# Performance work log

Hardware: AMD Instinct MI355X
Metric: run time of the kernel (lower is better)

## Reference

```python
import jax, jax.numpy as jnp
import numpy as np

FACTOR = 5  # sampling factor from __init__


def setup_inputs() -> dict:
    key = jax.random.key(0)
    k1, k2, k3, k4 = jax.random.split(key, 4)
    B, L, H, D = 4, 2048, 8, 64
    S = min(FACTOR * int(np.ceil(np.log(L))), L)  # U_part = 40
    return {
        "queries": jax.random.normal(k1, (B, L, H, D), jnp.float32),
        "keys": jax.random.normal(k2, (B, L, H, D), jnp.float32),
        "values": jax.random.normal(k3, (B, L, H, D), jnp.float32),
        "index_sample": jax.random.randint(k4, (L, S), 0, L, jnp.int32),
    }


def reference(queries, keys, values, index_sample):
    B, L_Q, H, D = queries.shape
    L_K = keys.shape[1]
    Q = jnp.transpose(queries, (0, 2, 1, 3))  # [B,H,L_Q,D]
    K = jnp.transpose(keys, (0, 2, 1, 3))     # [B,H,L_K,D]
    V = jnp.transpose(values, (0, 2, 1, 3))   # [B,H,L_K,D]

    u = min(FACTOR * int(np.ceil(np.log(L_Q))), L_Q)  # n_top

    # --- _prob_QK: sampled QK to score queries, then top-u query selection ---
    # K_sample[b,h,q,s,:] = K[b,h,index_sample[q,s],:]  -> [B,H,L_Q,S,D]
    K_sample = K[:, :, index_sample, :]
    Q_K_sample = jnp.einsum('bhqd,bhqsd->bhqs', Q, K_sample)  # [B,H,L_Q,S]
    M = Q_K_sample.max(-1) - Q_K_sample.sum(-1) / L_K         # sparsity measure
    _, M_top = jax.lax.top_k(M, u)                            # [B,H,u] query indices

    Q_reduce = jnp.take_along_axis(Q, M_top[..., None], axis=2)  # [B,H,u,D]
    scale = 1.0 / np.sqrt(D)
    scores = jnp.einsum('bhud,bhkd->bhuk', Q_reduce, K) * scale  # [B,H,u,L_K]

    # --- _update_context causal mask: rows are the FIRST u rows of the full
    # triu(L_Q,L_Q) mask (faithful to original, which does NOT reindex by M_top)
    causal = jnp.triu(jnp.ones((u, L_Q), dtype=bool), 1)
    scores = jnp.where(causal[None, None], -jnp.inf, scores)
    attn = jax.nn.softmax(scores, axis=-1)
    upd = jnp.einsum('bhuk,bhkd->bhud', attn, V)  # [B,H,u,D]

    # --- _get_initial_context (mask_flag=True): running cumsum of V ---
    context = jnp.cumsum(V, axis=2)  # [B,H,L_Q,D]

    # scatter-overwrite selected query positions
    b = jnp.arange(B)[:, None, None]
    h = jnp.arange(H)[None, :, None]
    context = context.at[b, h, M_top].set(upd)

    return jnp.transpose(context, (0, 2, 1, 3))  # [B,L_Q,H,D]
```

## Files before the change

kernel.cpp:

```cpp
#include <hip/hip_runtime.h>
#include <stdint.h>

constexpr int B = 4;
constexpr int L = 2048;
constexpr int H = 8;
constexpr int D = 64;
constexpr int S = 40;
constexpr int U = 40;
constexpr int HD = H * D;
constexpr int NSEG = 8;
constexpr int SEGL = L / NSEG;
constexpr int NC = 64;
constexpr int CL = L / NC;
constexpr int ROCT = 8;
constexpr int RPO = U / ROCT;

constexpr int NBLK_SCORES = B * L / 4;
constexpr int NBLK_CHUNK  = B * NC;
constexpr int NBLK_FLAG   = 64;

__device__ __forceinline__ unsigned mono(float v) {
    unsigned u = __float_as_uint(v);
    return (u & 0x80000000u) ? ~u : (u | 0x80000000u);
}

typedef float f4v __attribute__((ext_vector_type(4)));

__device__ __forceinline__ float4 ntload4(const float4* p) {
    f4v v = __builtin_nontemporal_load((const f4v*)p);
    return make_float4(v.x, v.y, v.z, v.w);
}

__global__ __launch_bounds__(256) void k_scores_chunks(
    const float4* __restrict__ Q4, const float4* __restrict__ K4,
    const int* __restrict__ idxs, const float* __restrict__ V,
    float* __restrict__ M, float* __restrict__ partial,
    int* __restrict__ flags)
{
    int i = blockIdx.x;

    if (i < NBLK_SCORES) {
        int xcd = i & 7;
        int b = xcd >> 1;
        int qc = (i >> 3) * 2 + (xcd & 1);
        int w = threadIdx.x >> 6;
        int lane = threadIdx.x & 63;
        int q = qc * 4 + w;
        int g = lane >> 4;
        int m = lane & 15;

        const float4* qrow = Q4 + (size_t)(b * L + q) * 128;
        float4 qa = ntload4(qrow + lane);
        float4 qb = ntload4(qrow + 64 + lane);

        int v_idx = idxs[q * S + (lane < S ? lane : 0)];

        const float4* kbase = K4 + (size_t)b * L * 128;
        float mxA = -INFINITY, smA = 0.f;
        float mxB = -INFINITY, smB = 0.f;
        #pragma unroll 8
        for (int s = 0; s < S; ++s) {
            int ki = __shfl(v_idx, s);
            const float4* krow = kbase + (size_t)ki * 128;
            float4 ka = krow[lane];
            float4 kb = krow[64 + lane];
            float dA = qa.x * ka.x + qa.y * ka.y + qa.z * ka.z + qa.w * ka.w;
            float dB = qb.x * kb.x + qb.y * kb.y + qb.z * kb.z + qb.w * kb.w;
            dA += __shfl_xor(dA, 1);  dB += __shfl_xor(dB, 1);
            dA += __shfl_xor(dA, 2);  dB += __shfl_xor(dB, 2);
            dA += __shfl_xor(dA, 4);  dB += __shfl_xor(dB, 4);
            dA += __shfl_xor(dA, 8);  dB += __shfl_xor(dB, 8);
            mxA = fmaxf(mxA, dA);  smA += dA;
            mxB = fmaxf(mxB, dB);  smB += dB;
        }
        if (m == 0) {
            M[(b * 8 + g) * L + q]       = mxA - smA * (1.0f / (float)L);
            M[(b * 8 + g + 4) * L + q]   = mxB - smB * (1.0f / (float)L);
        }
    } else if (i < NBLK_SCORES + NBLK_CHUNK) {
        int cidx = i - NBLK_SCORES;
        int b = cidx >> 6, c = cidx & 63;
        int t = threadIdx.x;
        const float* vp = V + ((size_t)(b * L + c * CL)) * HD;
        float s0 = 0.f, s1 = 0.f;
        #pragma unroll
        for (int l = 0; l < CL; ++l) {
            s0 += __builtin_nontemporal_load(vp + (size_t)l * HD + t);
            s1 += __builtin_nontemporal_load(vp + (size_t)l * HD + t + 256);
        }
        partial[((size_t)b * NC + c) * HD + t]       = s0;
        partial[((size_t)b * NC + c) * HD + t + 256] = s1;
    } else {
        int fidx = i - (NBLK_SCORES + NBLK_CHUNK);
        ((int4*)flags)[fidx * 256 + threadIdx.x] = make_int4(0, 0, 0, 0);
    }
}

__global__ __launch_bounds__(64) void k_seg_topk(
    const float* __restrict__ M, unsigned long long* __restrict__ cand)
{
    int blk = blockIdx.x;
    int bh = blk >> 3, seg = blk & 7;
    int lane = threadIdx.x;
    int j0 = seg * SEGL + lane * 4;

    float4 v = *(const float4*)(M + (size_t)bh * L + j0);
    unsigned m[4] = { mono(v.x), mono(v.y), mono(v.z), mono(v.w) };
    int rank[4] = { 0, 0, 0, 0 };

    #pragma unroll 4
    for (int src = 0; src < 64; ++src) {
        #pragma unroll
        for (int slot = 0; slot < 4; ++slot) {
            unsigned bm = __shfl(m[slot], src);
            int bj = src * 4 + slot;
            #pragma unroll
            for (int s = 0; s < 4; ++s) {
                int myj = lane * 4 + s;
                rank[s] += (bm > m[s]) || (bm == m[s] && bj < myj);
            }
        }
    }

    unsigned long long* out = cand + (size_t)blk * U;
    #pragma unroll
    for (int s = 0; s < 4; ++s)
        if (rank[s] < U)
            out[rank[s]] = ((unsigned long long)m[s] << 32)
                         | (unsigned)(~(unsigned)(j0 + s));
}

__global__ __launch_bounds__(512) void k_attn(
    const unsigned long long* __restrict__ cand, const float4* __restrict__ Q4,
    const float4* __restrict__ K4, const float4* __restrict__ V4,
    int* __restrict__ flags, float* __restrict__ upd)
{
    __shared__ unsigned long long cnd[NSEG * U];
    __shared__ int top_idx[U];
    __shared__ __align__(16) float Qs[RPO * 68];
    __shared__ __align__(16) float Kst[64 * 65];
    __shared__ __align__(16) float Vs[U * 68];
    __shared__ __align__(16) float Plds[RPO * 44];

    int blk = blockIdx.x;
    int bh = blk >> 3, oct = blk & 7;
    int b = bh >> 3, h = bh & 7;
    int tid = threadIdx.x;
    int wv = tid >> 6, lane = tid & 63;

    for (int t = tid; t < NSEG * U; t += 512)
        cnd[t] = cand[(size_t)bh * NSEG * U + t];
    __syncthreads();

    if (tid < NSEG * U) {
        unsigned long long ka = cnd[tid];
        int ra = 0;
        #pragma unroll 8
        for (int j = 0; j < NSEG * U; ++j) ra += (cnd[j] > ka);
        if (ra < U) top_idx[ra] = (int)(~(unsigned)ka);
    }
    __syncthreads();

    if (oct == 0 && tid < U) flags[bh * L + top_idx[tid]] = tid + 1;

    for (int i = tid; i < U * 16; i += 512) {
        int r = i >> 4, d4 = i & 15;
        size_t kvbase = ((size_t)(b * L + r) * H + h) * 16 + d4;
        float4 kv = K4[kvbase];
        Kst[(4 * d4 + 0) * 65 + r] = kv.x;
        Kst[(4 * d4 + 1) * 65 + r] = kv.y;
        Kst[(4 * d4 + 2) * 65 + r] = kv.z;
        Kst[(4 * d4 + 3) * 65 + r] = kv.w;
        *(float4*)(Vs + r * 68 + d4 * 4) = V4[kvbase];
    }
    if (tid < RPO * 16) {
        int rl = tid >> 4, d4 = tid & 15;
        int qg = top_idx[oct * RPO + rl];
        *(float4*)(Qs + rl * 68 + d4 * 4) =
            Q4[((size_t)(b * L + qg) * H + h) * 16 + d4];
    }
    __syncthreads();

    const float scale = 0.125f;
    if (wv < RPO) {
        int rg = oct * RPO + wv;
        int k = lane;
        float acc = 0.f;
        #pragma unroll
        for (int d0 = 0; d0 < D; d0 += 4) {
            float4 qv = *(const float4*)(Qs + wv * 68 + d0);
            acc += qv.x * Kst[(d0 + 0) * 65 + k];
            acc += qv.y * Kst[(d0 + 1) * 65 + k];
            acc += qv.z * Kst[(d0 + 2) * 65 + k];
            acc += qv.w * Kst[(d0 + 3) * 65 + k];
        }
        float sc = (k <= rg) ? acc * scale : -INFINITY;
        float mx = sc;
        #pragma unroll
        for (int off = 32; off >= 1; off >>= 1)
            mx = fmaxf(mx, __shfl_xor(mx, off));
        float e = __expf(sc - mx);
        float sum = e;
        #pragma unroll
        for (int off = 32; off >= 1; off >>= 1)
            sum += __shfl_xor(sum, off);
        float p = e / sum;
        if (k < U) Plds[wv * 44 + k] = p;
    }
    __syncthreads();

    if (tid < RPO * D) {
        int rl = tid >> 6, d = tid & 63;
        float acc = 0.f;
        #pragma unroll
        for (int kk = 0; kk < U; kk += 4) {
            float4 pv = *(const float4*)(Plds + rl * 44 + kk);
            acc += pv.x * Vs[(kk + 0) * 68 + d];
            acc += pv.y * Vs[(kk + 1) * 68 + d];
            acc += pv.z * Vs[(kk + 2) * 68 + d];
            acc += pv.w * Vs[(kk + 3) * 68 + d];
        }
        upd[((size_t)bh * U + oct * RPO + rl) * D + d] = acc;
    }
}

__global__ __launch_bounds__(512) void k_out(
    const float* __restrict__ V, const float* __restrict__ partial,
    const int* __restrict__ flags, const float* __restrict__ upd,
    float* __restrict__ out)
{
    int b = blockIdx.x >> 6;
    int c = blockIdx.x & 63;
    int hd = threadIdx.x;
    int h = hd >> 6, d = hd & 63;

    const float* pp = partial + (size_t)b * NC * HD + hd;
    float a0 = 0.f, a1 = 0.f, a2 = 0.f, a3 = 0.f;
    int j = 0;
    for (; j + 4 <= c; j += 4) {
        a0 += pp[(size_t)(j + 0) * HD];
        a1 += pp[(size_t)(j + 1) * HD];
        a2 += pp[(size_t)(j + 2) * HD];
        a3 += pp[(size_t)(j + 3) * HD];
    }
    for (; j < c; ++j) a0 += pp[(size_t)j * HD];
    float acc = (a0 + a1) + (a2 + a3);

    const float* vp = V + ((size_t)(b * L + c * CL)) * HD + hd;
    float*       op = out + ((size_t)(b * L + c * CL)) * HD + hd;
    const int*   fp = flags + (b * H + h) * L + c * CL;
    const float* up = upd + (size_t)(b * H + h) * U * D + d;

    #pragma unroll 4
    for (int l = 0; l < CL; ++l) {
        acc += vp[(size_t)l * HD];
        int f = fp[l];
        float o = f ? up[(size_t)(f - 1) * D] : acc;
        __builtin_nontemporal_store(o, op + (size_t)l * HD);
    }
}

extern "C" void kernel_launch(void* const* d_in, const int* in_sizes, int n_in,
                              void* d_out, int out_size, void* d_ws, size_t ws_size,
                              hipStream_t stream)
{
    const float* Q   = (const float*)d_in[0];
    const float* K   = (const float*)d_in[1];
    const float* V   = (const float*)d_in[2];
    const int*  idxs = (const int*)d_in[3];
    float* out = (float*)d_out;

    char* ws = (char*)d_ws;
    float* M        = (float*)(ws);
    int*   flags    = (int*)  (ws + 262144);
    float* upd      = (float*)(ws + 524288);
    float* partial  = (float*)(ws + 851968);
    unsigned long long* cand = (unsigned long long*)(ws + 1376256);

    k_scores_chunks<<<NBLK_SCORES + NBLK_CHUNK + NBLK_FLAG, 256, 0, stream>>>(
        (const float4*)Q, (const float4*)K, idxs, V, M, partial, flags);
    k_seg_topk <<<B * H * NSEG, 64, 0, stream>>>(M, cand);
    k_attn     <<<B * H * ROCT, 512, 0, stream>>>(cand, (const float4*)Q, (const float4*)K,
                                                  (const float4*)V, flags, upd);
    k_out      <<<B * NC,      512, 0, stream>>>(V, partial, flags, upd, out);
}
```

Baseline: 174.5 us.

## Fuse segment top-k into attention kernel and split sample loop across waves

The segmented top-k kernel is removed. Each of the 8 attention blocks per (b,h) now recomputes the 8 segment rankings itself from M, one wave per segment, writing candidates straight to shared memory. This drops one kernel launch and the candidate buffer round trip, at the cost of repeating the ranking work 8 times across blocks. Separately, the scoring kernel now splits the 40 samples across two waves per query, combining max and sum through shared memory. This doubles the block count to add memory-level parallelism on the gathered K rows.

```diff
diff --git a/kernel.cpp b/kernel.cpp
--- a/kernel.cpp
+++ b/kernel.cpp
@@ -14,8 +14,9 @@
 constexpr int CL = L / NC;
 constexpr int ROCT = 8;
 constexpr int RPO = U / ROCT;
-
-constexpr int NBLK_SCORES = B * L / 4;
+constexpr int SH = S / 2;
+
+constexpr int NBLK_SCORES = B * L / 2;
 constexpr int NBLK_CHUNK  = B * NC;
 constexpr int NBLK_FLAG   = 64;
 
@@ -31,7 +32,7 @@
     return make_float4(v.x, v.y, v.z, v.w);
 }
 
-__global__ __launch_bounds__(256) void k_scores_chunks(
+__global__ __launch_bounds__(256, 4) void k_scores_chunks(
     const float4* __restrict__ Q4, const float4* __restrict__ K4,
     const int* __restrict__ idxs, const float* __restrict__ V,
     float* __restrict__ M, float* __restrict__ partial,
@@ -40,12 +41,16 @@
     int i = blockIdx.x;
 
     if (i < NBLK_SCORES) {
+        __shared__ float red_mx[4][8];
+        __shared__ float red_sm[4][8];
+
         int xcd = i & 7;
         int b = xcd >> 1;
-        int qc = (i >> 3) * 2 + (xcd & 1);
+        int qp = (i >> 3) * 2 + (xcd & 1);
         int w = threadIdx.x >> 6;
         int lane = threadIdx.x & 63;
-        int q = qc * 4 + w;
+        int q = qp * 2 + (w >> 1);
+        int half = w & 1;
         int g = lane >> 4;
         int m = lane & 15;
 
@@ -53,13 +58,13 @@
         float4 qa = ntload4(qrow + lane);
         float4 qb = ntload4(qrow + 64 + lane);
 
-        int v_idx = idxs[q * S + (lane < S ? lane : 0)];
+        int v_idx = idxs[q * S + half * SH + (lane < SH ? lane : 0)];
 
         const float4* kbase = K4 + (size_t)b * L * 128;
         float mxA = -INFINITY, smA = 0.f;
         float mxB = -INFINITY, smB = 0.f;
-        #pragma unroll 8
-        for (int s = 0; s < S; ++s) {
+        #pragma unroll 10
+        for (int s = 0; s < SH; ++s) {
             int ki = __shfl(v_idx, s);
             const float4* krow = kbase + (size_t)ki * 128;
             float4 ka = krow[lane];
@@ -74,8 +79,16 @@
             mxB = fmaxf(mxB, dB);  smB += dB;
         }
         if (m == 0) {
-            M[(b * 8 + g) * L + q]       = mxA - smA * (1.0f / (float)L);
-            M[(b * 8 + g + 4) * L + q]   = mxB - smB * (1.0f / (float)L);
+            red_mx[w][g]     = mxA;  red_sm[w][g]     = smA;
+            red_mx[w][g + 4] = mxB;  red_sm[w][g + 4] = smB;
+        }
+        __syncthreads();
+        if (threadIdx.x < 16) {
+            int qi = threadIdx.x >> 3, h = threadIdx.x & 7;
+            int w0 = qi * 2;
+            float mx = fmaxf(red_mx[w0][h], red_mx[w0 + 1][h]);
+            float sm = red_sm[w0][h] + red_sm[w0 + 1][h];
+            M[(b * 8 + h) * L + (qp * 2 + qi)] = mx - sm * (1.0f / (float)L);
         }
     } else if (i < NBLK_SCORES + NBLK_CHUNK) {
         int cidx = i - NBLK_SCORES;
@@ -96,42 +109,8 @@
     }
 }
 
-__global__ __launch_bounds__(64) void k_seg_topk(
-    const float* __restrict__ M, unsigned long long* __restrict__ cand)
-{
-    int blk = blockIdx.x;
-    int bh = blk >> 3, seg = blk & 7;
-    int lane = threadIdx.x;
-    int j0 = seg * SEGL + lane * 4;
-
-    float4 v = *(const float4*)(M + (size_t)bh * L + j0);
-    unsigned m[4] = { mono(v.x), mono(v.y), mono(v.z), mono(v.w) };
-    int rank[4] = { 0, 0, 0, 0 };
-
-    #pragma unroll 4
-    for (int src = 0; src < 64; ++src) {
-        #pragma unroll
-        for (int slot = 0; slot < 4; ++slot) {
-            unsigned bm = __shfl(m[slot], src);
-            int bj = src * 4 + slot;
-            #pragma unroll
-            for (int s = 0; s < 4; ++s) {
-                int myj = lane * 4 + s;
-                rank[s] += (bm > m[s]) || (bm == m[s] && bj < myj);
-            }
-        }
-    }
-
-    unsigned long long* out = cand + (size_t)blk * U;
-    #pragma unroll
-    for (int s = 0; s < 4; ++s)
-        if (rank[s] < U)
-            out[rank[s]] = ((unsigned long long)m[s] << 32)
-                         | (unsigned)(~(unsigned)(j0 + s));
-}
-
-__global__ __launch_bounds__(512) void k_attn(
-    const unsigned long long* __restrict__ cand, const float4* __restrict__ Q4,
+__global__ __launch_bounds__(512) void k_topk_attn(
+    const float* __restrict__ M, const float4* __restrict__ Q4,
     const float4* __restrict__ K4, const float4* __restrict__ V4,
     int* __restrict__ flags, float* __restrict__ upd)
 {
@@ -148,8 +127,32 @@
     int tid = threadIdx.x;
     int wv = tid >> 6, lane = tid & 63;
 
-    for (int t = tid; t < NSEG * U; t += 512)
-        cnd[t] = cand[(size_t)bh * NSEG * U + t];
+    {
+        int seg = wv;
+        int j0 = seg * SEGL + lane * 4;
+        float4 v = *(const float4*)(M + (size_t)bh * L + j0);
+        unsigned m[4] = { mono(v.x), mono(v.y), mono(v.z), mono(v.w) };
+        int rank[4] = { 0, 0, 0, 0 };
+
+        #pragma unroll 4
+        for (int src = 0; src < 64; ++src) {
+            #pragma unroll
+            for (int slot = 0; slot < 4; ++slot) {
+                unsigned bm = __shfl(m[slot], src);
+                int bj = src * 4 + slot;
+                #pragma unroll
+                for (int s = 0; s < 4; ++s) {
+                    int myj = lane * 4 + s;
+                    rank[s] += (bm > m[s]) || (bm == m[s] && bj < myj);
+                }
+            }
+        }
+        #pragma unroll
+        for (int s = 0; s < 4; ++s)
+            if (rank[s] < U)
+                cnd[seg * U + rank[s]] = ((unsigned long long)m[s] << 32)
+                                       | (unsigned)(~(unsigned)(j0 + s));
+    }
     __syncthreads();
 
     if (tid < NSEG * U) {
@@ -275,12 +278,10 @@
     int*   flags    = (int*)  (ws + 262144);
     float* upd      = (float*)(ws + 524288);
     float* partial  = (float*)(ws + 851968);
-    unsigned long long* cand = (unsigned long long*)(ws + 1376256);
 
     k_scores_chunks<<<NBLK_SCORES + NBLK_CHUNK + NBLK_FLAG, 256, 0, stream>>>(
         (const float4*)Q, (const float4*)K, idxs, V, M, partial, flags);
-    k_seg_topk <<<B * H * NSEG, 64, 0, stream>>>(M, cand);
-    k_attn     <<<B * H * ROCT, 512, 0, stream>>>(cand, (const float4*)Q, (const float4*)K,
+    k_topk_attn<<<B * H * ROCT, 512, 0, stream>>>(M, (const float4*)Q, (const float4*)K,
                                                   (const float4*)V, flags, upd);
-    k_out      <<<B * NC,      512, 0, stream>>>(V, partial, flags, upd, out);
-}
+    k_out      <<<B * NC,       512, 0, stream>>>(V, partial, flags, upd, out);
+}
```

Result: no change. 176.5 us (+1.2%).
